# Optimization experiments

Hardware: AMD Instinct MI355X
Metric: run time of the kernel (lower is better)

## Reference

```python
import math
import jax, jax.numpy as jnp
import numpy as np

B, T, D = 4, 2048, 1024
H = 16
DK = D // H


def setup_inputs() -> dict:
    key = jax.random.key(0)
    ks = jax.random.split(key, 9)
    s = 1.0 / math.sqrt(D)
    return {
        "x": jax.random.normal(ks[0], (B, T, D), dtype=jnp.float32),
        "Wq": jax.random.normal(ks[1], (D, D), dtype=jnp.float32) * s,
        "bq": jax.random.normal(ks[2], (D,), dtype=jnp.float32) * s,
        "Wk": jax.random.normal(ks[3], (D, D), dtype=jnp.float32) * s,
        "bk": jax.random.normal(ks[4], (D,), dtype=jnp.float32) * s,
        "Wv": jax.random.normal(ks[5], (D, D), dtype=jnp.float32) * s,
        "bv": jax.random.normal(ks[6], (D,), dtype=jnp.float32) * s,
        "Wo": jax.random.normal(ks[7], (D, D), dtype=jnp.float32) * s,
        "bo": jax.random.normal(ks[8], (D,), dtype=jnp.float32) * s,
    }


def reference(x, Wq, bq, Wk, bk, Wv, bv, Wo, bo):
    Bx, Tx, C = x.shape
    # projections -> [B, H, T, d_k]
    q = (x @ Wq + bq).reshape(Bx, Tx, H, DK).transpose(0, 2, 1, 3)
    k = (x @ Wk + bk).reshape(Bx, Tx, H, DK).transpose(0, 2, 1, 3)
    v = (x @ Wv + bv).reshape(Bx, Tx, H, DK).transpose(0, 2, 1, 3)
    # scores [B, H, T, T], scaled
    scores = jnp.einsum("bhqd,bhkd->bhqk", q, k) / math.sqrt(DK)
    causal = jnp.tril(jnp.ones((Tx, Tx), dtype=bool))
    scores = jnp.where(causal[None, None, :, :], scores, -jnp.inf)
    attn = jax.nn.softmax(scores, axis=-1)  # dropout p=0.0 (eval)
    out = jnp.einsum("bhqk,bhkd->bhqd", attn, v)
    out = out.transpose(0, 2, 1, 3).reshape(Bx, Tx, C)
    return out @ Wo + bo
```

## Files before the change

kernel.cpp:

```cpp
#include <hip/hip_runtime.h>
#include <stdint.h>
#include <math.h>

typedef __attribute__((ext_vector_type(8))) __bf16 bf16x8;
typedef __attribute__((ext_vector_type(4))) __bf16 bf16x4;
typedef __attribute__((ext_vector_type(4))) float f32x4;
typedef __attribute__((ext_vector_type(4))) short short4v;

__device__ __forceinline__ void load_lds16(const void* g, void* l) {
  __builtin_amdgcn_global_load_lds((__attribute__((address_space(1))) void*)(g),
                                   (__attribute__((address_space(3))) void*)(l),
                                   16, 0, 0);
}

__device__ __forceinline__ uint32_t pack_bf2(float a, float b) {
  union { __bf16 h; uint16_t u; } x, y;
  x.h = (__bf16)a; y.h = (__bf16)b;
  return (uint32_t)x.u | ((uint32_t)y.u << 16);
}

__device__ __forceinline__ short4v mk4(uint32_t lo, uint32_t hi) {
  union { uint32_t d[2]; short4v v; } u;
  u.d[0] = lo; u.d[1] = hi;
  return u.v;
}

__device__ __forceinline__ f32x4 mfma16(short4v a, short4v b, f32x4 c) {
#if defined(__has_builtin) && __has_builtin(__builtin_amdgcn_mfma_f32_16x16x16bf16_1k)
  return __builtin_amdgcn_mfma_f32_16x16x16bf16_1k(a, b, c, 0, 0, 0);
#else
  asm volatile("v_mfma_f32_16x16x16_bf16 %0, %1, %2, %0"
               : "+v"(c) : "v"(a), "v"(b));
  return c;
#endif
}

__global__ __launch_bounds__(256)
void convert_x(const float* __restrict__ xf, __bf16* __restrict__ xb) {
  const size_t i = ((size_t)blockIdx.x * 256 + threadIdx.x) * 8;
  const float4 u0 = *(const float4*)(xf + i);
  const float4 u1 = *(const float4*)(xf + i + 4);
  bf16x8 v;
  v[0] = (__bf16)u0.x; v[1] = (__bf16)u0.y; v[2] = (__bf16)u0.z; v[3] = (__bf16)u0.w;
  v[4] = (__bf16)u1.x; v[5] = (__bf16)u1.y; v[6] = (__bf16)u1.z; v[7] = (__bf16)u1.w;
  *(bf16x8*)&xb[i] = v;
}

__global__ __launch_bounds__(256)
void prep_weights(const float* __restrict__ Wq, const float* __restrict__ Wk,
                  const float* __restrict__ Wv, const float* __restrict__ Wo,
                  const float* __restrict__ bq, const float* __restrict__ bk,
                  const float* __restrict__ bv, const float* __restrict__ bo,
                  __bf16* __restrict__ Bt1, __bf16* __restrict__ Bt2,
                  float* __restrict__ bqkv, float* __restrict__ bo_f) {
  const int m = blockIdx.z;
  const float* W = (m == 0) ? Wq : (m == 1) ? Wk : (m == 2) ? Wv : Wo;
  __bf16* Out = (m == 3) ? Bt2 : Bt1 + (size_t)m * 1024 * 1024;
  const int kt = blockIdx.x * 64, nt = blockIdx.y * 64;
  __shared__ __bf16 tile[64 * 68];
  const int t = threadIdx.x;
#pragma unroll
  for (int i = 0; i < 16; i++) {
    int e = i * 256 + t;
    int r = e >> 6, c = e & 63;
    tile[r * 68 + c] = (__bf16)W[(size_t)(kt + r) * 1024 + nt + c];
  }
  __syncthreads();
#pragma unroll
  for (int i = 0; i < 16; i++) {
    int e = i * 256 + t;
    int r = e >> 6, c = e & 63;
    Out[(size_t)(nt + r) * 1024 + kt + c] = tile[c * 68 + r];
  }
  if (blockIdx.x == 0 && blockIdx.y == 0) {
    if (m < 3) {
      const float* bsrc = (m == 0) ? bq : (m == 1) ? bk : bv;
      for (int i = t; i < 1024; i += 256) bqkv[m * 1024 + i] = bsrc[i];
    } else {
      for (int i = t; i < 1024; i += 256) bo_f[i] = bo[i];
    }
  }
}

__global__ __launch_bounds__(512)
void gemm256(const __bf16* __restrict__ A, const __bf16* __restrict__ Bt,
             const float* __restrict__ bias, void* __restrict__ Cv,
             int out_f32, int M, int N, int K) {
  __shared__ __align__(16) __bf16 As[2][256 * 64];
  __shared__ __align__(16) __bf16 Bs[2][256 * 64];
  const int t = threadIdx.x, lane = t & 63, wave = t >> 6;
  const int wm = wave >> 2, wn = wave & 3;
  const int fm = lane & 15, fq = lane >> 4;
  const int bm = blockIdx.x * 256, bn = blockIdx.y * 256;

  const int srow = t >> 3;
  const int scol = ((t & 7) ^ (srow & 7)) << 3;
  const __bf16* Ag = A + (size_t)(bm + srow) * K + scol;
  const __bf16* Bg = Bt + (size_t)(bn + srow) * K + scol;
  const size_t rstep = (size_t)64 * K;

  f32x4 acc[8][4] = {};
  const int nkt = K >> 6;
  int cur = 0;

#define GSTAGE(KT, BUF)                                                   \
  {                                                                       \
    const size_t ko = (size_t)(KT) * 64;                                  \
    load_lds16(Ag + ko,             &As[BUF][t * 8]);                     \
    load_lds16(Ag + ko + rstep,     &As[BUF][4096 + t * 8]);              \
    load_lds16(Ag + ko + 2 * rstep, &As[BUF][8192 + t * 8]);              \
    load_lds16(Ag + ko + 3 * rstep, &As[BUF][12288 + t * 8]);             \
    load_lds16(Bg + ko,             &Bs[BUF][t * 8]);                     \
    load_lds16(Bg + ko + rstep,     &Bs[BUF][4096 + t * 8]);              \
    load_lds16(Bg + ko + 2 * rstep, &Bs[BUF][8192 + t * 8]);              \
    load_lds16(Bg + ko + 3 * rstep, &Bs[BUF][12288 + t * 8]);             \
  }

  GSTAGE(0, 0);
  for (int kt = 0; kt < nkt; kt++) {
    if (kt + 1 < nkt) {
      GSTAGE(kt + 1, cur ^ 1);
      asm volatile("s_waitcnt vmcnt(8)" ::: "memory");
    } else {
      asm volatile("s_waitcnt vmcnt(0)" ::: "memory");
    }
    __builtin_amdgcn_s_barrier();
    __builtin_amdgcn_sched_barrier(0);
    const __bf16* Ac = As[cur];
    const __bf16* Bc = Bs[cur];
#pragma unroll
    for (int ks = 0; ks < 2; ks++) {
      bf16x8 af[8], bf[4];
#pragma unroll
      for (int mi = 0; mi < 8; mi++) {
        const int row = wm * 128 + mi * 16 + fm;
        af[mi] = *(const bf16x8*)&Ac[row * 64 + ((((ks << 2) | fq) ^ (fm & 7)) << 3)];
      }
#pragma unroll
      for (int ni = 0; ni < 4; ni++) {
        const int row = wn * 64 + ni * 16 + fm;
        bf[ni] = *(const bf16x8*)&Bc[row * 64 + ((((ks << 2) | fq) ^ (fm & 7)) << 3)];
      }
      __builtin_amdgcn_s_setprio(1);
#pragma unroll
      for (int mi = 0; mi < 8; mi++)
#pragma unroll
        for (int ni = 0; ni < 4; ni++)
          acc[mi][ni] = __builtin_amdgcn_mfma_f32_16x16x32_bf16(af[mi], bf[ni],
                                                                acc[mi][ni], 0, 0, 0);
      __builtin_amdgcn_s_setprio(0);
    }
    __builtin_amdgcn_sched_barrier(0);
    __builtin_amdgcn_s_barrier();
    cur ^= 1;
  }
#undef GSTAGE

#pragma unroll
  for (int ni = 0; ni < 4; ni++) {
    const int col = bn + wn * 64 + ni * 16 + fm;
    const float bvv = bias[col];
#pragma unroll
    for (int mi = 0; mi < 8; mi++)
#pragma unroll
      for (int r = 0; r < 4; r++) {
        const int row = bm + wm * 128 + mi * 16 + fq * 4 + r;
        const float val = acc[mi][ni][r] + bvv;
        if (out_f32) ((float*)Cv)[(size_t)row * N + col] = val;
        else ((__bf16*)Cv)[(size_t)row * N + col] = (__bf16)val;
      }
  }
}

__global__ __launch_bounds__(256)
void transpose_v(const __bf16* __restrict__ QKV, __bf16* __restrict__ Vt) {
  const int tt = blockIdx.x;
  const int bh = blockIdx.y;
  const int b = bh >> 4, h = bh & 15;
  __shared__ __bf16 tile[64 * 68];
  const int t = threadIdx.x;
#pragma unroll
  for (int i = 0; i < 16; i++) {
    int e = i * 256 + t;
    int tok = e >> 6, dk = e & 63;
    tile[tok * 68 + dk] =
        QKV[((size_t)b * 2048 + tt * 64 + tok) * 3072 + 2048 + h * 64 + dk];
  }
  __syncthreads();
#pragma unroll
  for (int i = 0; i < 16; i++) {
    int e = i * 256 + t;
    int dk = e >> 6, tok = e & 63;
    Vt[((size_t)bh * 64 + dk) * 2048 + tt * 64 + tok] = tile[tok * 68 + dk];
  }
}

__global__ __launch_bounds__(512)
void flash_attn(const __bf16* __restrict__ QKV, const __bf16* __restrict__ Vt,
                __bf16* __restrict__ O) {
  const int y = blockIdx.y;
  const int p = (y < 4) ? y : 11 - y;
  const int qhi = 15 - p, qlo = p;
  const int bh = blockIdx.x;
  const int b = bh >> 4, h = bh & 15;
  __shared__ __align__(16) __bf16 Ks[2][64 * 64];
  __shared__ __align__(16) __bf16 Vs[2][64 * 64];
  const int t = threadIdx.x, lane = t & 63, wave = t >> 6;
  const int fm = lane & 15, fq = lane >> 4;
  const int tok0 = t >> 3;
  const int csw = ((t & 7) ^ (tok0 & 7)) << 3;
  const int swb = (fm & 7) << 4;
  const int rb0 = (((fq << 4)) ^ swb) >> 1;
  const int rb1 = ((64 + (fq << 4)) ^ swb) >> 1;
  int voff[4];
#pragma unroll
  for (int nt = 0; nt < 4; nt++)
    voff[nt] = (((((nt << 1) | (fq >> 1))) ^ (fm & 7)) << 3) | ((fq & 1) << 2);

  const size_t kbase = ((size_t)b * 2048) * 3072 + 1024 + h * 64;
  const size_t vbase = (size_t)bh * 64 * 2048;
  const int nkt = 2 * qhi + 2;
  const int qmin[2] = {qhi * 128 + wave * 16, qlo * 128 + wave * 16};
  const float SC = 0.18033688011112042f;
  const float THR_RAW = 44.3614195558365f;

  bf16x8 qf[2][2];
#pragma unroll
  for (int mi = 0; mi < 2; mi++) {
    const size_t qrow = ((size_t)b * 2048 + qmin[mi] + fm) * 3072 + h * 64;
    qf[mi][0] = *(const bf16x8*)&QKV[qrow + fq * 8];
    qf[mi][1] = *(const bf16x8*)&QKV[qrow + 32 + fq * 8];
  }

  const short4v ones4 = {(short)0x3F80, (short)0x3F80, (short)0x3F80, (short)0x3F80};

  f32x4 o_acc[2][4] = {};
  float m_i[2] = {-1e30f, -1e30f}, l_i[2] = {0.f, 0.f};

#define STAGE(KT, BUF)                                                          \
  {                                                                             \
    const int kb2 = (KT) * 64;                                                  \
    load_lds16(&QKV[kbase + (size_t)(kb2 + tok0) * 3072 + csw],                 \
               &Ks[BUF][t * 8]);                                                \
    load_lds16(&Vt[vbase + (size_t)tok0 * 2048 + kb2 + csw],                    \
               &Vs[BUF][t * 8]);                                                \
  }

  STAGE(0, 0);
  __syncthreads();
  int cur = 0;

  for (int kt = 0; kt < nkt; kt++) {
    const int kb = kt * 64;
    if (kt + 1 < nkt) STAGE(kt + 1, cur ^ 1);

    const bool act0 = (kb <= qmin[0] + 15);
    const bool act1 = (kb <= qmin[1] + 15);
    if (act0) {
      const __bf16* Kc = Ks[cur];
      const __bf16* Vc = Vs[cur];

      f32x4 s[2][4];
      __builtin_amdgcn_s_setprio(1);
#pragma unroll
      for (int nt = 0; nt < 4; nt++) {
        const bf16x8 kf0 = *(const bf16x8*)&Kc[(nt * 16 + fm) * 64 + rb0];
        const bf16x8 kf1 = *(const bf16x8*)&Kc[(nt * 16 + fm) * 64 + rb1];
        {
          f32x4 z = {};
          z = __builtin_amdgcn_mfma_f32_16x16x32_bf16(kf0, qf[0][0], z, 0, 0, 0);
          z = __builtin_amdgcn_mfma_f32_16x16x32_bf16(kf1, qf[0][1], z, 0, 0, 0);
          s[0][nt] = z;
        }
        if (act1) {
          f32x4 z = {};
          z = __builtin_amdgcn_mfma_f32_16x16x32_bf16(kf0, qf[1][0], z, 0, 0, 0);
          z = __builtin_amdgcn_mfma_f32_16x16x32_bf16(kf1, qf[1][1], z, 0, 0, 0);
          s[1][nt] = z;
        }
      }
      __builtin_amdgcn_s_setprio(0);

#pragma unroll
      for (int mi = 0; mi < 2; mi++) {
        if (mi == 1 && !act1) continue;
        if (kb + 63 > qmin[mi]) {
          const int qq = qmin[mi] + fm;
#pragma unroll
          for (int nt = 0; nt < 4; nt++) {
            const int kk = kb + nt * 16 + fq * 4;
#pragma unroll
            for (int r = 0; r < 4; r++)
              if (kk + r > qq) s[mi][nt][r] = -1e30f;
          }
        }
      }

#pragma unroll
      for (int mi = 0; mi < 2; mi++) {
        if (mi == 1 && !act1) continue;

        float a = fmaxf(fmaxf(s[mi][0][0], s[mi][0][1]),
                        fmaxf(s[mi][0][2], s[mi][0][3]));
#pragma unroll
        for (int nt = 1; nt < 4; nt++)
          a = fmaxf(a, fmaxf(fmaxf(s[mi][nt][0], s[mi][nt][1]),
                             fmaxf(s[mi][nt][2], s[mi][nt][3])));
        a = fmaxf(a, __shfl_xor(a, 16, 64));
        a = fmaxf(a, __shfl_xor(a, 32, 64));
        const float rmax = a;

        if (!__all(rmax - m_i[mi] <= THR_RAW)) {
          const float mn = fmaxf(m_i[mi], rmax);
          const float al = exp2f(SC * (m_i[mi] - mn));
          m_i[mi] = mn;
          l_i[mi] *= al;
#pragma unroll
          for (int dt = 0; dt < 4; dt++)
#pragma unroll
            for (int r = 0; r < 4; r++) o_acc[mi][dt][r] *= al;
        }

        short4v pb[4];
        const float msc = -SC * m_i[mi];
#pragma unroll
        for (int nt = 0; nt < 4; nt++) {
          const float p0 = exp2f(fmaf(s[mi][nt][0], SC, msc));
          const float p1 = exp2f(fmaf(s[mi][nt][1], SC, msc));
          const float p2 = exp2f(fmaf(s[mi][nt][2], SC, msc));
          const float p3 = exp2f(fmaf(s[mi][nt][3], SC, msc));
          pb[nt] = mk4(pack_bf2(p0, p1), pack_bf2(p2, p3));
        }

        f32x4 rs = {};
#pragma unroll
        for (int nt = 0; nt < 4; nt++) rs = mfma16(ones4, pb[nt], rs);

        __builtin_amdgcn_s_setprio(1);
#pragma unroll
        for (int dt = 0; dt < 4; dt++) {
          const int rowb = (dt * 16 + fm) * 64;
          f32x4 o = o_acc[mi][dt];
#pragma unroll
          for (int nt = 0; nt < 4; nt++) {
            const short4v vf = *(const short4v*)&Vc[rowb + voff[nt]];
            o = mfma16(vf, pb[nt], o);
          }
          o_acc[mi][dt] = o;
        }
        __builtin_amdgcn_s_setprio(0);

        l_i[mi] += rs[0];
      }
    }

    __syncthreads();
    cur ^= 1;
  }

#pragma unroll
  for (int mi = 0; mi < 2; mi++) {
    const float linv = 1.f / l_i[mi];
    const size_t orow = (size_t)b * 2048 + qmin[mi] + fm;
#pragma unroll
    for (int dt = 0; dt < 4; dt++) {
      bf16x4 w;
#pragma unroll
      for (int r = 0; r < 4; r++) w[r] = (__bf16)(o_acc[mi][dt][r] * linv);
      *(bf16x4*)&O[orow * 1024 + h * 64 + dt * 16 + fq * 4] = w;
    }
  }
#undef STAGE
}

extern "C" void kernel_launch(void* const* d_in, const int* in_sizes, int n_in,
                              void* d_out, int out_size, void* d_ws, size_t ws_size,
                              hipStream_t stream) {
  const float* x = (const float*)d_in[0];
  const float* Wq = (const float*)d_in[1];
  const float* bq = (const float*)d_in[2];
  const float* Wk = (const float*)d_in[3];
  const float* bk = (const float*)d_in[4];
  const float* Wv = (const float*)d_in[5];
  const float* bv = (const float*)d_in[6];
  const float* Wo = (const float*)d_in[7];
  const float* bo = (const float*)d_in[8];

  char* ws = (char*)d_ws;
  __bf16* Bt1 = (__bf16*)(ws);
  __bf16* Bt2 = (__bf16*)(ws + 6291456);
  float* bqkv = (float*)(ws + 8388608);
  float* bo_f = (float*)(ws + 8400896);
  __bf16* QKV = (__bf16*)(ws + 8405504);
  __bf16* Vt = (__bf16*)(ws + 58737152);
  __bf16* Xb = (__bf16*)(ws + 75514368);
  __bf16* Ow = Xb;

  hipLaunchKernelGGL(convert_x, dim3(4096), dim3(256), 0, stream, x, Xb);
  hipLaunchKernelGGL(prep_weights, dim3(16, 16, 4), dim3(256), 0, stream,
                     Wq, Wk, Wv, Wo, bq, bk, bv, bo, Bt1, Bt2, bqkv, bo_f);
  hipLaunchKernelGGL(gemm256, dim3(32, 12), dim3(512), 0, stream,
                     Xb, Bt1, bqkv, (void*)QKV, 0, 8192, 3072, 1024);
  hipLaunchKernelGGL(transpose_v, dim3(32, 64), dim3(256), 0, stream, QKV, Vt);
  hipLaunchKernelGGL(flash_attn, dim3(64, 8), dim3(512), 0, stream, QKV, Vt, Ow);
  hipLaunchKernelGGL(gemm256, dim3(32, 4), dim3(512), 0, stream,
                     Ow, Bt2, bo_f, d_out, 1, 8192, 1024, 1024);
}
```

Measured before the change: 333.0 us.

## Interleave GEMM global-to-LDS loads with MFMA phases in finer-grained stages

Restructures the 256x256 GEMM main loop into four compute phases per K-tile, each issuing part of the next tile's A loads or the B loads two tiles ahead between LDS fragment reads and MFMA blocks. B is prefetched one extra stage early into the buffer being consumed. The aim is to spread memory traffic across the iteration and hide load latency behind MFMA work instead of issuing all loads at once. The cost is many more barriers per iteration and a delicate buffer-reuse ordering that could race if the waitcnt accounting is wrong.

```diff
diff --git a/kernel.cpp b/kernel.cpp
--- a/kernel.cpp
+++ b/kernel.cpp
@@ -97,64 +97,104 @@
   const int scol = ((t & 7) ^ (srow & 7)) << 3;
   const __bf16* Ag = A + (size_t)(bm + srow) * K + scol;
   const __bf16* Bg = Bt + (size_t)(bn + srow) * K + scol;
-  const size_t rstep = (size_t)64 * K;
+
+  const int kc0 = ((fq ^ (fm & 7)) << 3);
+  const int kc1 = (((4 | fq) ^ (fm & 7)) << 3);
 
   f32x4 acc[8][4] = {};
   const int nkt = K >> 6;
-  int cur = 0;
-
-#define GSTAGE(KT, BUF)                                                   \
-  {                                                                       \
-    const size_t ko = (size_t)(KT) * 64;                                  \
-    load_lds16(Ag + ko,             &As[BUF][t * 8]);                     \
-    load_lds16(Ag + ko + rstep,     &As[BUF][4096 + t * 8]);              \
-    load_lds16(Ag + ko + 2 * rstep, &As[BUF][8192 + t * 8]);              \
-    load_lds16(Ag + ko + 3 * rstep, &As[BUF][12288 + t * 8]);             \
-    load_lds16(Bg + ko,             &Bs[BUF][t * 8]);                     \
-    load_lds16(Bg + ko + rstep,     &Bs[BUF][4096 + t * 8]);              \
-    load_lds16(Bg + ko + 2 * rstep, &Bs[BUF][8192 + t * 8]);              \
-    load_lds16(Bg + ko + 3 * rstep, &Bs[BUF][12288 + t * 8]);             \
-  }
-
-  GSTAGE(0, 0);
-  for (int kt = 0; kt < nkt; kt++) {
-    if (kt + 1 < nkt) {
-      GSTAGE(kt + 1, cur ^ 1);
-      asm volatile("s_waitcnt vmcnt(8)" ::: "memory");
-    } else {
-      asm volatile("s_waitcnt vmcnt(0)" ::: "memory");
-    }
-    __builtin_amdgcn_s_barrier();
-    __builtin_amdgcn_sched_barrier(0);
-    const __bf16* Ac = As[cur];
-    const __bf16* Bc = Bs[cur];
-#pragma unroll
-    for (int ks = 0; ks < 2; ks++) {
-      bf16x8 af[8], bf[4];
-#pragma unroll
-      for (int mi = 0; mi < 8; mi++) {
-        const int row = wm * 128 + mi * 16 + fm;
-        af[mi] = *(const bf16x8*)&Ac[row * 64 + ((((ks << 2) | fq) ^ (fm & 7)) << 3)];
-      }
-#pragma unroll
-      for (int ni = 0; ni < 4; ni++) {
-        const int row = wn * 64 + ni * 16 + fm;
-        bf[ni] = *(const bf16x8*)&Bc[row * 64 + ((((ks << 2) | fq) ^ (fm & 7)) << 3)];
-      }
-      __builtin_amdgcn_s_setprio(1);
-#pragma unroll
-      for (int mi = 0; mi < 8; mi++)
-#pragma unroll
-        for (int ni = 0; ni < 4; ni++)
-          acc[mi][ni] = __builtin_amdgcn_mfma_f32_16x16x32_bf16(af[mi], bf[ni],
-                                                                acc[mi][ni], 0, 0, 0);
-      __builtin_amdgcn_s_setprio(0);
-    }
-    __builtin_amdgcn_sched_barrier(0);
-    __builtin_amdgcn_s_barrier();
-    cur ^= 1;
-  }
-#undef GSTAGE
+
+#define SA_UNIT(TT, BUF, U)                                                  \
+  load_lds16(Ag + (size_t)(U) * 64 * K + (size_t)(TT) * 64,                  \
+             &As[BUF][(U) * 4096 + t * 8])
+#define SB_UNIT(TT, BUF, U)                                                  \
+  load_lds16(Bg + (size_t)(U) * 64 * K + (size_t)(TT) * 64,                  \
+             &Bs[BUF][(U) * 4096 + t * 8])
+
+  SA_UNIT(0, 0, 0); SA_UNIT(0, 0, 1); SA_UNIT(0, 0, 2); SA_UNIT(0, 0, 3);
+  SB_UNIT(0, 0, 0); SB_UNIT(0, 0, 1); SB_UNIT(0, 0, 2); SB_UNIT(0, 0, 3);
+  if (nkt > 1) {
+    SB_UNIT(1, 1, 0); SB_UNIT(1, 1, 1); SB_UNIT(1, 1, 2); SB_UNIT(1, 1, 3);
+    asm volatile("s_waitcnt vmcnt(4)" ::: "memory");
+  } else {
+    asm volatile("s_waitcnt vmcnt(0)" ::: "memory");
+  }
+  __builtin_amdgcn_s_barrier();
+
+  for (int j = 0; j < nkt; ++j) {
+    const int c = j & 1;
+    const __bf16* Ac = As[c];
+    const __bf16* Bc = Bs[c];
+    const int ar0 = (wm * 128 + fm) * 64;
+    const int br0 = (wn * 64 + fm) * 64;
+    bf16x8 afl[4], afh[4], bf0[4], bf1[4];
+
+#pragma unroll
+    for (int mi = 0; mi < 4; mi++) afl[mi] = *(const bf16x8*)&Ac[ar0 + mi * 1024 + kc0];
+#pragma unroll
+    for (int ni = 0; ni < 4; ni++) bf0[ni] = *(const bf16x8*)&Bc[br0 + ni * 1024 + kc0];
+    if (j + 1 < nkt) { SA_UNIT(j + 1, c ^ 1, 0); SA_UNIT(j + 1, c ^ 1, 2); }
+    __builtin_amdgcn_s_barrier();
+    __builtin_amdgcn_s_setprio(1);
+#pragma unroll
+    for (int mi = 0; mi < 4; mi++)
+#pragma unroll
+      for (int ni = 0; ni < 4; ni++)
+        acc[mi][ni] = __builtin_amdgcn_mfma_f32_16x16x32_bf16(afl[mi], bf0[ni],
+                                                              acc[mi][ni], 0, 0, 0);
+    __builtin_amdgcn_s_setprio(0);
+    __builtin_amdgcn_s_barrier();
+
+#pragma unroll
+    for (int mi = 0; mi < 4; mi++) afl[mi] = *(const bf16x8*)&Ac[ar0 + mi * 1024 + kc1];
+#pragma unroll
+    for (int ni = 0; ni < 4; ni++) bf1[ni] = *(const bf16x8*)&Bc[br0 + ni * 1024 + kc1];
+    if (j + 1 < nkt) { SA_UNIT(j + 1, c ^ 1, 1); SA_UNIT(j + 1, c ^ 1, 3); }
+    __builtin_amdgcn_s_barrier();
+    __builtin_amdgcn_s_setprio(1);
+#pragma unroll
+    for (int mi = 0; mi < 4; mi++)
+#pragma unroll
+      for (int ni = 0; ni < 4; ni++)
+        acc[mi][ni] = __builtin_amdgcn_mfma_f32_16x16x32_bf16(afl[mi], bf1[ni],
+                                                              acc[mi][ni], 0, 0, 0);
+    __builtin_amdgcn_s_setprio(0);
+    __builtin_amdgcn_s_barrier();
+
+#pragma unroll
+    for (int mi = 0; mi < 4; mi++)
+      afh[mi] = *(const bf16x8*)&Ac[ar0 + (mi + 4) * 1024 + kc0];
+    if (j + 2 < nkt) { SB_UNIT(j + 2, c, 0); SB_UNIT(j + 2, c, 1); }
+    __builtin_amdgcn_s_barrier();
+    __builtin_amdgcn_s_setprio(1);
+#pragma unroll
+    for (int mi = 0; mi < 4; mi++)
+#pragma unroll
+      for (int ni = 0; ni < 4; ni++)
+        acc[mi + 4][ni] = __builtin_amdgcn_mfma_f32_16x16x32_bf16(afh[mi], bf0[ni],
+                                                                  acc[mi + 4][ni], 0, 0, 0);
+    __builtin_amdgcn_s_setprio(0);
+    __builtin_amdgcn_s_barrier();
+
+#pragma unroll
+    for (int mi = 0; mi < 4; mi++)
+      afh[mi] = *(const bf16x8*)&Ac[ar0 + (mi + 4) * 1024 + kc1];
+    if (j + 2 < nkt) { SB_UNIT(j + 2, c, 2); SB_UNIT(j + 2, c, 3); }
+    __builtin_amdgcn_s_barrier();
+    __builtin_amdgcn_s_setprio(1);
+#pragma unroll
+    for (int mi = 0; mi < 4; mi++)
+#pragma unroll
+      for (int ni = 0; ni < 4; ni++)
+        acc[mi + 4][ni] = __builtin_amdgcn_mfma_f32_16x16x32_bf16(afh[mi], bf1[ni],
+                                                                  acc[mi + 4][ni], 0, 0, 0);
+    __builtin_amdgcn_s_setprio(0);
+    if (j + 2 < nkt) asm volatile("s_waitcnt vmcnt(4)" ::: "memory");
+    else asm volatile("s_waitcnt vmcnt(0)" ::: "memory");
+    __builtin_amdgcn_s_barrier();
+  }
+#undef SA_UNIT
+#undef SB_UNIT
 
 #pragma unroll
   for (int ni = 0; ni < 4; ni++) {
```

Measured after the change: 323.5 us. 1.03x faster.
